# Optimization experiments

Measured on AMD Instinct MI355X. Metric: run time of the kernel, lower is better.

The kernel has to match this reference:

```python
import jax, jax.numpy as jnp
import numpy as np

NUM_CATEGORIES = 10
LMB = 0.5


def conv2d_relu(x, w, b):
    # x: NHWC, w: HWIO, stride 1, SAME padding, relu
    y = jax.lax.conv_general_dilated(x, w, (1, 1), 'SAME',
                                     dimension_numbers=('NHWC', 'HWIO', 'NHWC'))
    return jax.nn.relu(y + b)


def maxpool2(x):
    return jax.lax.reduce_window(x, -jnp.inf, jax.lax.max,
                                 (1, 2, 2, 1), (1, 2, 2, 1), 'VALID')


def compute_mask(x, lmb):
    # x: (b, h, w, c), h == w. Per-(batch, channel) spatial argmax -> L1 pyramid mask.
    b, h, w, c = x.shape
    flat = jnp.transpose(x, (0, 3, 1, 2)).reshape(b, c, h * w)
    idx = jnp.argmax(flat, axis=-1)                      # (b, c)
    scale = (h - 1.0) / 2.0
    mu_x = (idx // w).astype(x.dtype) / scale - 1.0      # row coord in [-1, 1]
    mu_y = (idx % w).astype(x.dtype) / scale - 1.0       # col coord in [-1, 1]
    lin = jnp.linspace(-1.0, 1.0, h).astype(x.dtype)
    dist = (jnp.abs(lin[None, :, None, None] - mu_x[:, None, None, :])
            + jnp.abs(lin[None, None, :, None] - mu_y[:, None, None, :]))  # (b,h,w,c)
    return jnp.maximum(1.0 - lmb * dist, -1.0)


def setup_inputs() -> dict:
    key = jax.random.key(0)
    ks = jax.random.split(key, 10)
    B, H, W = 32, 128, 128
    inputs = jax.random.normal(ks[0], (B, H, W, 1), dtype=jnp.float32)
    labels = jax.random.randint(ks[1], (B,), 0, NUM_CATEGORIES, dtype=jnp.int64)
    conv1_w = jax.random.normal(ks[2], (3, 3, 1, 32), dtype=jnp.float32) * 0.1
    conv1_b = jnp.zeros((32,), dtype=jnp.float32)
    conv2_w = jax.random.normal(ks[3], (3, 3, 32, 64), dtype=jnp.float32) * 0.05
    conv2_b = jnp.zeros((64,), dtype=jnp.float32)
    flat_dim = (H // 4) * (W // 4) * 64  # 65536
    dense1_w = jax.random.normal(ks[4], (flat_dim, 1024), dtype=jnp.float32) * 0.01
    dense1_b = jnp.zeros((1024,), dtype=jnp.float32)
    dense2_w = jax.random.normal(ks[5], (1024, 10), dtype=jnp.float32) * 0.05
    dense2_b = jnp.zeros((10,), dtype=jnp.float32)
    return {'inputs': inputs, 'labels': labels,
            'conv1_w': conv1_w, 'conv1_b': conv1_b,
            'conv2_w': conv2_w, 'conv2_b': conv2_b,
            'dense1_w': dense1_w, 'dense1_b': dense1_b,
            'dense2_w': dense2_w, 'dense2_b': dense2_b}


def reference(inputs, labels, conv1_w, conv1_b, conv2_w, conv2_b,
              dense1_w, dense1_b, dense2_w, dense2_b):
    conv1_out = conv2d_relu(inputs, conv1_w, conv1_b)          # (B,128,128,32)
    conv1_pool = maxpool2(conv1_out)                           # (B,64,64,32)
    conv2_out = conv2d_relu(conv1_pool, conv2_w, conv2_b)      # (B,64,64,64)
    conv2_masked = conv2_out * compute_mask(conv2_out, LMB)
    conv2_pool = maxpool2(jax.nn.relu(conv2_masked))           # (B,32,32,64)
    flattened = conv2_pool.reshape(conv2_pool.shape[0], -1)    # (B,65536)
    dense_out = jax.nn.relu(flattened @ dense1_w + dense1_b)
    # Keras Dropout is identity at inference (training=False default)
    logits = dense_out @ dense2_w + dense2_b                   # (B,10)

    # Per-category scatter accumulation (segment-sum over batch)
    per_sample = jnp.sum(conv2_out, axis=(1, 2))               # (B,64)
    sum_act = jax.ops.segment_sum(per_sample, labels, num_segments=NUM_CATEGORIES)
    counts = jax.ops.segment_sum(jnp.ones_like(labels, dtype=jnp.float32),
                                 labels, num_segments=NUM_CATEGORIES)
    avg_act = sum_act / counts[:, None]                        # (10,64)
    filter_categories = jnp.argmax(avg_act, axis=0)            # (64,)
    return (logits, conv2_pool, filter_categories)
```

## Files before the change

### kernel.cpp

```cpp
#include <hip/hip_runtime.h>

__global__ void k_conv1_pool(const float* __restrict__ x, const float* __restrict__ w,
                             const float* __restrict__ bias, float* __restrict__ out) {
    int t = blockIdx.x * blockDim.x + threadIdx.x;
    int c  = t & 31;
    int pw = (t >> 5) & 63;
    int ph = (t >> 11) & 63;
    int n  = t >> 17;
    float wv[9];
#pragma unroll
    for (int i = 0; i < 9; ++i) wv[i] = w[i * 32 + c];
    float b = bias[c];
    float patch[4][4];
#pragma unroll
    for (int r = 0; r < 4; ++r) {
        int gr = 2 * ph - 1 + r;
#pragma unroll
        for (int col = 0; col < 4; ++col) {
            int gc = 2 * pw - 1 + col;
            patch[r][col] = (gr >= 0 && gr < 128 && gc >= 0 && gc < 128)
                ? x[(n * 128 + gr) * 128 + gc] : 0.f;
        }
    }
    float m = 0.f;
#pragma unroll
    for (int dh = 0; dh < 2; ++dh)
#pragma unroll
    for (int dw = 0; dw < 2; ++dw) {
        float s = b;
#pragma unroll
        for (int kh = 0; kh < 3; ++kh)
#pragma unroll
        for (int kw = 0; kw < 3; ++kw)
            s = fmaf(patch[dh + kh][dw + kw], wv[kh * 3 + kw], s);
        m = fmaxf(m, s);
    }
    out[t] = m;
}

__global__ void k_w2t(const float* __restrict__ w2, float* __restrict__ w2t) {
    int t = blockIdx.x * blockDim.x + threadIdx.x;
    if (t >= 18432) return;
    int i   = t & 3;
    int co  = (t >> 2) & 63;
    int ci4 = (t >> 8) & 7;
    int p   = t >> 11;
    w2t[t] = w2[(p * 32 + ci4 * 4 + i) * 64 + co];
}

__global__ void __launch_bounds__(256, 2)
k_conv2(const float* __restrict__ in, const float* __restrict__ w2t,
        const float* __restrict__ bias, float* __restrict__ out) {
    __shared__ __align__(16) float lds[18 * 10 * 32];
    int bid = blockIdx.x;
    int n = bid >> 5;
    int tile = bid & 31;
    int r0b = (tile >> 3) * 16;
    int c0b = (tile & 7) * 8;
    int tid = threadIdx.x;
    for (int i = tid; i < 5760; i += 256) {
        int ci = i & 31;
        int cr = i >> 5;
        int col = cr % 10;
        int row = cr / 10;
        int gr = r0b - 1 + row;
        int gc = c0b - 1 + col;
        float v = 0.f;
        if (gr >= 0 && gr < 64 && gc >= 0 && gc < 64)
            v = in[((n * 64 + gr) * 64 + gc) * 32 + ci];
        lds[i] = v;
    }
    __syncthreads();
    int co = tid & 63;
    int rp = tid >> 6;
    float bb = bias[co];
    const float* wbase = w2t + co * 4;
    const float* lbase = lds + rp * 4 * 320;
    float acc[4][8];
#pragma unroll
    for (int r = 0; r < 4; ++r)
#pragma unroll
        for (int c = 0; c < 8; ++c) acc[r][c] = bb;

#pragma unroll
    for (int q = 0; q < 6; ++q) {
        const int r_lo = (q > 2) ? (q - 2) : 0;
        for (int ci4 = 0; ci4 < 8; ++ci4) {
            float4 wreg[9];
#pragma unroll
            for (int r = 0; r < 4; ++r) {
                int kh = q - r;
                if (kh < 0 || kh > 2) continue;
#pragma unroll
                for (int kw = 0; kw < 3; ++kw)
                    wreg[(r - r_lo) * 3 + kw] =
                        *(const float4*)&wbase[((kh * 3 + kw) * 8 + ci4) * 256];
            }
            float4 v[10];
#pragma unroll
            for (int j = 0; j < 10; ++j)
                v[j] = *(const float4*)&lbase[q * 320 + j * 32 + ci4 * 4];
#pragma unroll
            for (int r = 0; r < 4; ++r) {
                int kh = q - r;
                if (kh < 0 || kh > 2) continue;
#pragma unroll
                for (int kw = 0; kw < 3; ++kw) {
                    float4 wv = wreg[(r - r_lo) * 3 + kw];
#pragma unroll
                    for (int c = 0; c < 8; ++c) {
                        float4 xv = v[c + kw];
                        float a = acc[r][c];
                        a = fmaf(xv.x, wv.x, a);
                        a = fmaf(xv.y, wv.y, a);
                        a = fmaf(xv.z, wv.z, a);
                        a = fmaf(xv.w, wv.w, a);
                        acc[r][c] = a;
                    }
                }
            }
        }
    }
#pragma unroll
    for (int r = 0; r < 4; ++r) {
        int gr = r0b + rp * 4 + r;
#pragma unroll
        for (int c = 0; c < 8; ++c) {
            int gc = c0b + c;
            out[((n * 64 + gr) * 64 + gc) * 64 + co] = fmaxf(acc[r][c], 0.f);
        }
    }
}

__global__ void k_argmax_A(const float* __restrict__ conv2, float* __restrict__ abest,
                           int* __restrict__ aidx, float* __restrict__ asum) {
    int n = blockIdx.x, part = blockIdx.y;
    int tid = threadIdx.x;
    int c = tid & 63, sub = tid >> 6;
    const float* base = conv2 + (size_t)n * 4096 * 64;
    int p0 = part * 256 + sub * 64;
    float best = -1e30f; int bi = p0; float s = 0.f;
    for (int i = 0; i < 64; ++i) {
        int p = p0 + i;
        float v = base[(size_t)p * 64 + c];
        s += v;
        if (v > best) { best = v; bi = p; }
    }
    __shared__ float sb[256], ss[256];
    __shared__ int sidx[256];
    sb[tid] = best; ss[tid] = s; sidx[tid] = bi;
    __syncthreads();
    if (sub == 0) {
        for (int pp = 1; pp < 4; ++pp) {
            float v = sb[pp * 64 + c];
            if (v > best) { best = v; bi = sidx[pp * 64 + c]; }
            s += ss[pp * 64 + c];
        }
        int o = (n * 16 + part) * 64 + c;
        abest[o] = best; aidx[o] = bi; asum[o] = s;
    }
}

__global__ void k_argmax_B(const float* __restrict__ abest, const int* __restrict__ aidx,
                           const float* __restrict__ asum, int* __restrict__ idx,
                           float* __restrict__ psum) {
    int n = blockIdx.x;
    int c = threadIdx.x;
    float best = -1e30f; int bi = 0; float s = 0.f;
    for (int part = 0; part < 16; ++part) {
        int o = (n * 16 + part) * 64 + c;
        float v = abest[o];
        s += asum[o];
        if (v > best) { best = v; bi = aidx[o]; }
    }
    idx[n * 64 + c] = bi;
    psum[n * 64 + c] = s;
}

__global__ void k_mask_pool(const float* __restrict__ conv2, const int* __restrict__ idx,
                            float* __restrict__ out) {
    int t = blockIdx.x * blockDim.x + threadIdx.x;
    int c  = t & 63;
    int pw = (t >> 6) & 31;
    int ph = (t >> 11) & 31;
    int n  = t >> 16;
    int id = idx[n * 64 + c];
    float ih = (float)(id >> 6);
    float iw = (float)(id & 63);
    float m = 0.f;
#pragma unroll
    for (int dh = 0; dh < 2; ++dh) {
#pragma unroll
        for (int dw = 0; dw < 2; ++dw) {
            int h = 2 * ph + dh, w = 2 * pw + dw;
            float d = (fabsf((float)h - ih) + fabsf((float)w - iw)) * (1.0f / 31.5f);
            float mask = fmaxf(1.0f - 0.5f * d, -1.0f);
            float v = conv2[(((size_t)n * 64 + h) * 64 + w) * 64 + c] * mask;
            m = fmaxf(m, v);
        }
    }
    out[t] = m;
}

__global__ void __launch_bounds__(256, 4)
k_dense1_partial(const float* __restrict__ xflat,
                 const float* __restrict__ w1,
                 float* __restrict__ partial) {
    __shared__ float xs[32 * 256];
    int chunk = blockIdx.x;
    int jg = blockIdx.y;
    int tid = threadIdx.x;
    int k0 = chunk * 256;
    for (int i = tid; i < 2048; i += 256) {
        int n = i >> 6, kq = i & 63;
        *(float4*)&xs[n * 256 + kq * 4] =
            *(const float4*)&xflat[(size_t)n * 65536 + k0 + kq * 4];
    }
    __syncthreads();
    int g  = tid >> 6;
    int jt = tid & 63;
    int j0 = jg * 256 + jt * 4;
    float acc[8][4];
#pragma unroll
    for (int n = 0; n < 8; ++n)
#pragma unroll
        for (int j = 0; j < 4; ++j) acc[n][j] = 0.f;
    const float* wp = w1 + (size_t)k0 * 1024 + j0;
    const float* xb = xs + g * 8 * 256;
    float4 wv[4], wn[4];
#pragma unroll
    for (int i = 0; i < 4; ++i) wv[i] = *(const float4*)&wp[(size_t)i * 1024];
    for (int k4 = 0; k4 < 64; ++k4) {
        int k = k4 * 4;
        int kpre = (k4 < 63) ? (k + 4) : 0;
#pragma unroll
        for (int i = 0; i < 4; ++i)
            wn[i] = *(const float4*)&wp[(size_t)(kpre + i) * 1024];
#pragma unroll
        for (int n = 0; n < 8; ++n) {
            float4 xv = *(const float4*)&xb[n * 256 + k];
#pragma unroll
            for (int j = 0; j < 4; ++j) {
                float a = acc[n][j];
                a = fmaf(xv.x, ((const float*)&wv[0])[j], a);
                a = fmaf(xv.y, ((const float*)&wv[1])[j], a);
                a = fmaf(xv.z, ((const float*)&wv[2])[j], a);
                a = fmaf(xv.w, ((const float*)&wv[3])[j], a);
                acc[n][j] = a;
            }
        }
#pragma unroll
        for (int i = 0; i < 4; ++i) wv[i] = wn[i];
    }
#pragma unroll
    for (int n = 0; n < 8; ++n) {
        int gn = g * 8 + n;
        *(float4*)&partial[((size_t)chunk * 32 + gn) * 1024 + j0] =
            make_float4(acc[n][0], acc[n][1], acc[n][2], acc[n][3]);
    }
}

__global__ void k_dense1_reduce(const float* __restrict__ partial, const float* __restrict__ b,
                                float* __restrict__ dout) {
    int t = blockIdx.x * blockDim.x + threadIdx.x;
    int n = t >> 10, j = t & 1023;
    float s = b[j];
    for (int ch = 0; ch < 256; ++ch)
        s += partial[((size_t)ch * 32 + n) * 1024 + j];
    dout[t] = fmaxf(s, 0.f);
}

__global__ void k_dense2(const float* __restrict__ dout, const float* __restrict__ w,
                         const float* __restrict__ b, float* __restrict__ logits) {
    int bid = blockIdx.x;
    int n = bid / 10, j = bid % 10;
    int lane = threadIdx.x;
    float s = 0.f;
    for (int k = lane; k < 1024; k += 64)
        s = fmaf(dout[n * 1024 + k], w[k * 10 + j], s);
#pragma unroll
    for (int off = 32; off > 0; off >>= 1)
        s += __shfl_down(s, off);
    if (lane == 0) logits[n * 10 + j] = s + b[j];
}

__global__ void k_filter_cat(const float* __restrict__ psum, const int* __restrict__ labels,
                             float* __restrict__ out) {
    int c = threadIdx.x;
    float sums[10]; int cnt[10];
#pragma unroll
    for (int i = 0; i < 10; ++i) { sums[i] = 0.f; cnt[i] = 0; }
    for (int bb = 0; bb < 32; ++bb) {
        int l = labels[bb];
        sums[l] += psum[bb * 64 + c];
        cnt[l]++;
    }
    int best_i = 0; float best = -1e30f;
    for (int i = 0; i < 10; ++i) {
        float v = sums[i] / (float)cnt[i];
        if (v != v) { best_i = i; break; }
        if (v > best) { best = v; best_i = i; }
    }
    out[c] = (float)best_i;
}

extern "C" void kernel_launch(void* const* d_in, const int* in_sizes, int n_in,
                              void* d_out, int out_size, void* d_ws, size_t ws_size,
                              hipStream_t stream) {
    const float* x    = (const float*)d_in[0];
    const int* labels = (const int*)d_in[1];
    const float* c1w  = (const float*)d_in[2];
    const float* c1b  = (const float*)d_in[3];
    const float* c2w  = (const float*)d_in[4];
    const float* c2b  = (const float*)d_in[5];
    const float* d1w  = (const float*)d_in[6];
    const float* d1b  = (const float*)d_in[7];
    const float* d2w  = (const float*)d_in[8];
    const float* d2b  = (const float*)d_in[9];
    float* out = (float*)d_out;
    float* ws  = (float*)d_ws;

    float* pool1   = ws;
    float* conv2o  = ws + 4194304;
    float* partial = conv2o;
    float* w2t     = ws + 12582912;
    int*   idx     = (int*)(ws + 12601344);
    float* psum    = ws + 12603392;
    float* abest   = ws + 12605440;
    int*   aidx    = (int*)(ws + 12638208);
    float* asum    = ws + 12670976;
    float* dense1o = ws + 12703744;

    float* logits = out;
    float* pool2  = out + 320;
    float* fcat   = out + 320 + 2097152;

    k_w2t<<<72, 256, 0, stream>>>(c2w, w2t);
    k_conv1_pool<<<16384, 256, 0, stream>>>(x, c1w, c1b, pool1);
    k_conv2<<<1024, 256, 0, stream>>>(pool1, w2t, c2b, conv2o);
    dim3 ga(32, 16);
    k_argmax_A<<<ga, 256, 0, stream>>>(conv2o, abest, aidx, asum);
    k_argmax_B<<<32, 64, 0, stream>>>(abest, aidx, asum, idx, psum);
    k_mask_pool<<<8192, 256, 0, stream>>>(conv2o, idx, pool2);
    dim3 g5(256, 4);
    k_dense1_partial<<<g5, 256, 0, stream>>>(pool2, d1w, partial);
    k_dense1_reduce<<<128, 256, 0, stream>>>(partial, d1b, dense1o);
    k_dense2<<<320, 64, 0, stream>>>(dense1o, d2w, d2b, logits);
    k_filter_cat<<<1, 64, 0, stream>>>(psum, labels, fcat);
}
```

Before: 539.0 us.

## Fuse per-channel argmax and sum reduction into conv2 epilogue

Each conv2 block now computes a per-channel running max, argmax index and sum over its output tile while the results are still in registers. It reduces across the four row-groups in LDS and writes one partial per tile. A small combine kernel then merges the 32 tile partials per image. This drops the separate argmax pass that re-read the whole 32 MB conv2 output, at the cost of extra LDS, a barrier and a few registers in conv2, which could affect its occupancy.

After: 621.2 us. +15.2%, slower.

```diff
diff --git a/kernel.cpp b/kernel.cpp
--- a/kernel.cpp
+++ b/kernel.cpp
@@ -50,8 +50,11 @@
 
 __global__ void __launch_bounds__(256, 2)
 k_conv2(const float* __restrict__ in, const float* __restrict__ w2t,
-        const float* __restrict__ bias, float* __restrict__ out) {
+        const float* __restrict__ bias, float* __restrict__ out,
+        float* __restrict__ tbest, int* __restrict__ tidx, float* __restrict__ tsum) {
     __shared__ __align__(16) float lds[18 * 10 * 32];
+    __shared__ float sb[256], ssum[256];
+    __shared__ int sidx[256];
     int bid = blockIdx.x;
     int n = bid >> 5;
     int tile = bid & 31;
@@ -121,57 +124,44 @@
             }
         }
     }
+    float best = -1e30f; int bi = 0; float s = 0.f;
 #pragma unroll
     for (int r = 0; r < 4; ++r) {
         int gr = r0b + rp * 4 + r;
 #pragma unroll
         for (int c = 0; c < 8; ++c) {
             int gc = c0b + c;
-            out[((n * 64 + gr) * 64 + gc) * 64 + co] = fmaxf(acc[r][c], 0.f);
-        }
-    }
-}
-
-__global__ void k_argmax_A(const float* __restrict__ conv2, float* __restrict__ abest,
-                           int* __restrict__ aidx, float* __restrict__ asum) {
-    int n = blockIdx.x, part = blockIdx.y;
-    int tid = threadIdx.x;
-    int c = tid & 63, sub = tid >> 6;
-    const float* base = conv2 + (size_t)n * 4096 * 64;
-    int p0 = part * 256 + sub * 64;
-    float best = -1e30f; int bi = p0; float s = 0.f;
-    for (int i = 0; i < 64; ++i) {
-        int p = p0 + i;
-        float v = base[(size_t)p * 64 + c];
-        s += v;
-        if (v > best) { best = v; bi = p; }
-    }
-    __shared__ float sb[256], ss[256];
-    __shared__ int sidx[256];
-    sb[tid] = best; ss[tid] = s; sidx[tid] = bi;
+            float v = fmaxf(acc[r][c], 0.f);
+            out[((n * 64 + gr) * 64 + gc) * 64 + co] = v;
+            s += v;
+            int p = gr * 64 + gc;
+            if (v > best || (v == best && p < bi)) { best = v; bi = p; }
+        }
+    }
+    sb[tid] = best; sidx[tid] = bi; ssum[tid] = s;
     __syncthreads();
-    if (sub == 0) {
+    if (rp == 0) {
         for (int pp = 1; pp < 4; ++pp) {
-            float v = sb[pp * 64 + c];
-            if (v > best) { best = v; bi = sidx[pp * 64 + c]; }
-            s += ss[pp * 64 + c];
-        }
-        int o = (n * 16 + part) * 64 + c;
-        abest[o] = best; aidx[o] = bi; asum[o] = s;
-    }
-}
-
-__global__ void k_argmax_B(const float* __restrict__ abest, const int* __restrict__ aidx,
-                           const float* __restrict__ asum, int* __restrict__ idx,
-                           float* __restrict__ psum) {
+            float v = sb[pp * 64 + co]; int ii = sidx[pp * 64 + co];
+            if (v > best || (v == best && ii < bi)) { best = v; bi = ii; }
+            s += ssum[pp * 64 + co];
+        }
+        int o = (n * 32 + tile) * 64 + co;
+        tbest[o] = best; tidx[o] = bi; tsum[o] = s;
+    }
+}
+
+__global__ void k_combine(const float* __restrict__ tbest, const int* __restrict__ tidx,
+                          const float* __restrict__ tsum, int* __restrict__ idx,
+                          float* __restrict__ psum) {
     int n = blockIdx.x;
     int c = threadIdx.x;
     float best = -1e30f; int bi = 0; float s = 0.f;
-    for (int part = 0; part < 16; ++part) {
-        int o = (n * 16 + part) * 64 + c;
-        float v = abest[o];
-        s += asum[o];
-        if (v > best) { best = v; bi = aidx[o]; }
+    for (int t = 0; t < 32; ++t) {
+        int o = (n * 32 + t) * 64 + c;
+        float v = tbest[o]; int ii = tidx[o];
+        s += tsum[o];
+        if (v > best || (v == best && ii < bi)) { best = v; bi = ii; }
     }
     idx[n * 64 + c] = bi;
     psum[n * 64 + c] = s;
@@ -326,10 +316,10 @@
     float* w2t     = ws + 12582912;
     int*   idx     = (int*)(ws + 12601344);
     float* psum    = ws + 12603392;
-    float* abest   = ws + 12605440;
-    int*   aidx    = (int*)(ws + 12638208);
-    float* asum    = ws + 12670976;
-    float* dense1o = ws + 12703744;
+    float* tbest   = ws + 12605440;
+    int*   tidx    = (int*)(ws + 12670976);
+    float* tsum    = ws + 12736512;
+    float* dense1o = ws + 12802048;
 
     float* logits = out;
     float* pool2  = out + 320;
@@ -337,10 +327,8 @@
 
     k_w2t<<<72, 256, 0, stream>>>(c2w, w2t);
     k_conv1_pool<<<16384, 256, 0, stream>>>(x, c1w, c1b, pool1);
-    k_conv2<<<1024, 256, 0, stream>>>(pool1, w2t, c2b, conv2o);
-    dim3 ga(32, 16);
-    k_argmax_A<<<ga, 256, 0, stream>>>(conv2o, abest, aidx, asum);
-    k_argmax_B<<<32, 64, 0, stream>>>(abest, aidx, asum, idx, psum);
+    k_conv2<<<1024, 256, 0, stream>>>(pool1, w2t, c2b, conv2o, tbest, tidx, tsum);
+    k_combine<<<32, 64, 0, stream>>>(tbest, tidx, tsum, idx, psum);
     k_mask_pool<<<8192, 256, 0, stream>>>(conv2o, idx, pool2);
     dim3 g5(256, 4);
     k_dense1_partial<<<g5, 256, 0, stream>>>(pool2, d1w, partial);
```
